# Kernel optimization log

Measured on AMD Instinct MI355X. Metric: run time of the kernel, lower is better.

The kernel has to match this reference:

```python
import jax, jax.numpy as jnp
import numpy as np

B, T, C = 4, 2048, 1024
H = 16
HD = C // H  # 64


def setup_inputs() -> dict:
    key = jax.random.key(0)
    k1, k2, k3 = jax.random.split(key, 3)
    x = jax.random.normal(k1, (B, T, C), dtype=jnp.float32)
    # learned params (torch Linear y = x @ W.T stored here as [in, out])
    Wqkv = jax.random.normal(k2, (C, 3 * C), dtype=jnp.float32) * (C ** -0.5)
    Wout = jax.random.normal(k3, (C, C), dtype=jnp.float32) * (C ** -0.5)
    bout = jnp.zeros((C,), dtype=jnp.float32)
    causal_mask = jnp.tril(jnp.ones((1, 1, T, T), dtype=bool))
    return {"x": x, "causal_mask": causal_mask, "Wqkv": Wqkv, "Wout": Wout, "bout": bout}


def reference(x, causal_mask, Wqkv, Wout, bout):
    b, t, c = x.shape
    scale = HD ** -0.5
    qkv = x @ Wqkv  # [B,T,3C]
    q, k, v = jnp.split(qkv, 3, axis=-1)
    # [B,T,C] -> [B,H,T,hd]
    q = q.reshape(b, t, H, HD).transpose(0, 2, 1, 3)
    k = k.reshape(b, t, H, HD).transpose(0, 2, 1, 3)
    v = v.reshape(b, t, H, HD).transpose(0, 2, 1, 3)
    att = jnp.einsum("bhqd,bhkd->bhqk", q, k) * scale  # [B,H,T,T]
    att = jnp.where(causal_mask, att, -jnp.inf)
    att = jax.nn.softmax(att, axis=-1)
    # dropout in eval mode == identity
    out = jnp.einsum("bhqk,bhkd->bhqd", att, v)  # [B,H,T,hd]
    out = out.transpose(0, 2, 1, 3).reshape(b, t, c)
    return out @ Wout + bout


if __name__ == "__main__":
    inp = setup_inputs()
    y = jax.jit(reference)(**inp)
    print(y.shape, y.dtype)
```

## Files before the change

kernel.cpp:

```cpp
#include <hip/hip_runtime.h>
#include <hip/hip_bf16.h>
#include <stdint.h>


typedef __bf16 bf16;
typedef __bf16 bf16x4 __attribute__((ext_vector_type(4)));
typedef __bf16 bf16x8 __attribute__((ext_vector_type(8)));
typedef float floatx4 __attribute__((ext_vector_type(4)));

#define MFMA16(a, b, c) __builtin_amdgcn_mfma_f32_16x16x32_bf16(a, b, c, 0, 0, 0)

#if defined(__has_builtin)
#if __has_builtin(__builtin_amdgcn_global_load_lds)
#define HAS_GLL 1
#endif
#endif

#ifdef HAS_GLL
__device__ __forceinline__ void gll16(const bf16* g, bf16* l) {
  __builtin_amdgcn_global_load_lds(
      (const __attribute__((address_space(1))) unsigned int*)g,
      (__attribute__((address_space(3))) unsigned int*)l, 16, 0, 0);
}
#endif

__global__ __launch_bounds__(256)
void convert_x(const float* __restrict__ in, bf16* __restrict__ out) {
  const size_t i = (size_t)blockIdx.x * 256 + threadIdx.x;
  const float4* p = (const float4*)in + i * 2;
  float4 a = p[0], b = p[1];
  bf16x8 v;
  v[0] = (bf16)a.x; v[1] = (bf16)a.y; v[2] = (bf16)a.z; v[3] = (bf16)a.w;
  v[4] = (bf16)b.x; v[5] = (bf16)b.y; v[6] = (bf16)b.z; v[7] = (bf16)b.w;
  *((bf16x8*)out + i) = v;
}

__global__ __launch_bounds__(256)
void transpose_w(const float* __restrict__ W, bf16* __restrict__ Wt, int K, int N) {
  __shared__ bf16 tile[32][33];
  const int k0 = blockIdx.y * 32, n0 = blockIdx.x * 32;
  const int t = threadIdx.x;
  {
    const int r = t >> 3, c4 = (t & 7) * 4;
    float4 v = *(const float4*)(W + (size_t)(k0 + r) * N + n0 + c4);
    tile[r][c4 + 0] = (bf16)v.x;
    tile[r][c4 + 1] = (bf16)v.y;
    tile[r][c4 + 2] = (bf16)v.z;
    tile[r][c4 + 3] = (bf16)v.w;
  }
  __syncthreads();
  {
    const int nr = t >> 3, kc = (t & 7) * 4;
    bf16x4 o;
#pragma unroll
    for (int j = 0; j < 4; ++j) o[j] = tile[kc + j][nr];
    *(bf16x4*)(Wt + (size_t)(n0 + nr) * K + k0 + kc) = o;
  }
}

__global__ __launch_bounds__(256)
void vtrans(const bf16* __restrict__ qkv, bf16* __restrict__ vtp) {
  __shared__ bf16 tile[64][72];
  const int t = threadIdx.x;
  const int kb = blockIdx.x * 64;
  const int bh = blockIdx.y;
  const int b = bh >> 4, h = bh & 15;
  const bf16* Vp = qkv + (size_t)b * 2048 * 3072 + 2048 + h * 64;
#pragma unroll
  for (int i = 0; i < 2; ++i) {
    const int c = t + 256 * i, kk = c >> 3, dg = c & 7;
    *(bf16x8*)(&tile[kk][dg * 8]) =
        *(const bf16x8*)(Vp + (size_t)(kb + kk) * 3072 + dg * 8);
  }
  __syncthreads();
#pragma unroll
  for (int i = 0; i < 2; ++i) {
    const int c = t + 256 * i, d = c >> 3, g = c & 7;
    bf16x8 v;
#pragma unroll
    for (int j = 0; j < 8; ++j) v[j] = tile[g * 8 + j][d];
    *(bf16x8*)(vtp + ((size_t)bh * 64 + d) * 2048 + kb + g * 8) = v;
  }
}

template <bool OUT_BF16>
__global__ __launch_bounds__(256, 3)
void gemm_bt(const bf16* __restrict__ A, const bf16* __restrict__ Bt,
             const float* __restrict__ bias, void* __restrict__ Cv,
             int M, int N, int K) {
  __shared__ __align__(16) bf16 As[128 * 64];
  __shared__ __align__(16) bf16 Bs[128 * 64];

  const int t = threadIdx.x, lane = t & 63, w = t >> 6;
  const int m_ = lane & 15, quad = lane >> 4;
  const int wm = w >> 1, wn = w & 1;
  const int m0 = blockIdx.y * 128, n0 = blockIdx.x * 128;

  floatx4 acc[4][4];
#pragma unroll
  for (int i = 0; i < 4; ++i)
#pragma unroll
    for (int j = 0; j < 4; ++j) {
      floatx4 z = {0.f, 0.f, 0.f, 0.f};
      acc[i][j] = z;
    }

  for (int k0 = 0; k0 < K; k0 += 64) {
#pragma unroll
    for (int i = 0; i < 4; ++i) {
      const int R0 = i * 32 + w * 8;
      const int R = R0 + (lane >> 3);
      const int sg = (lane & 7) ^ (R & 7);
      const bf16* ga = A + (size_t)(m0 + R) * K + k0 + sg * 8;
      const bf16* gb = Bt + (size_t)(n0 + R) * K + k0 + sg * 8;
#ifdef HAS_GLL
      gll16(ga, As + (size_t)R0 * 64);
      gll16(gb, Bs + (size_t)R0 * 64);
#else
      *(bf16x8*)(As + (size_t)R * 64 + (lane & 7) * 8) = *(const bf16x8*)ga;
      *(bf16x8*)(Bs + (size_t)R * 64 + (lane & 7) * 8) = *(const bf16x8*)gb;
#endif
    }
    __syncthreads();

#pragma unroll
    for (int kc = 0; kc < 2; ++kc) {
      bf16x8 af[4], bfr[4];
#pragma unroll
      for (int mt = 0; mt < 4; ++mt) {
        const int r = wm * 64 + mt * 16 + m_;
        const int slot = ((kc << 2) | quad) ^ (r & 7);
        af[mt] = *(const bf16x8*)(As + (size_t)r * 64 + slot * 8);
      }
#pragma unroll
      for (int nt = 0; nt < 4; ++nt) {
        const int rn = wn * 64 + nt * 16 + m_;
        const int slot = ((kc << 2) | quad) ^ (rn & 7);
        bfr[nt] = *(const bf16x8*)(Bs + (size_t)rn * 64 + slot * 8);
      }
#pragma unroll
      for (int mt = 0; mt < 4; ++mt)
#pragma unroll
        for (int nt = 0; nt < 4; ++nt)
          acc[mt][nt] = MFMA16(af[mt], bfr[nt], acc[mt][nt]);
    }
    __syncthreads();
  }

#pragma unroll
  for (int mt = 0; mt < 4; ++mt)
#pragma unroll
    for (int nt = 0; nt < 4; ++nt) {
      const int col = n0 + wn * 64 + nt * 16 + m_;
      const float bv = bias ? bias[col] : 0.f;
#pragma unroll
      for (int r = 0; r < 4; ++r) {
        const int row = m0 + wm * 64 + mt * 16 + quad * 4 + r;
        const float val = acc[mt][nt][r] + bv;
        if (OUT_BF16)
          ((bf16*)Cv)[(size_t)row * N + col] = (bf16)val;
        else
          ((float*)Cv)[(size_t)row * N + col] = val;
      }
    }
}

__global__ __launch_bounds__(256, 2)
void attn_fwd(const bf16* __restrict__ qkv, const bf16* __restrict__ vtp,
              bf16* __restrict__ attnout) {
  constexpr int KS = 72;
  __shared__ __align__(16) bf16 Ks[64 * KS];
  __shared__ __align__(16) bf16 VT[64 * KS];
  __shared__ __align__(16) bf16 Pl[128 * KS];

  const int t = threadIdx.x, lane = t & 63, w = t >> 6;
  const int m_ = lane & 15, quad = lane >> 4;
  const int pb = blockIdx.x;
  const int bh = blockIdx.y;
  const int b = bh >> 4, h = bh & 15;
  const int srcbase = (lane & 48) + ((lane & 48) >> 2);

  const bf16* base = qkv + (size_t)b * 2048 * 3072;
  const bf16* Qp = base + h * 64;
  const bf16* Kp = base + 1024 + h * 64;
  const bf16* Vt = vtp + (size_t)bh * 64 * 2048;

#pragma unroll
  for (int pass = 0; pass < 2; ++pass) {
    const int qb = pass ? (15 - pb) : pb;
    const int q0w = qb * 128 + w * 32;

    bf16x8 qf[2][2];
#pragma unroll
    for (int mt = 0; mt < 2; ++mt)
#pragma unroll
      for (int kc = 0; kc < 2; ++kc)
        qf[mt][kc] = *(const bf16x8*)(Qp + (size_t)(q0w + mt * 16 + m_) * 3072 +
                                      kc * 32 + quad * 8);

    floatx4 o[2][4];
#pragma unroll
    for (int mt = 0; mt < 2; ++mt)
#pragma unroll
      for (int nt = 0; nt < 4; ++nt) {
        floatx4 z = {0.f, 0.f, 0.f, 0.f};
        o[mt][nt] = z;
      }
    float mrow[2] = {-1e30f, -1e30f}, lrow[2] = {0.f, 0.f};

    const int nch = 2 * qb + 2;
    for (int ch = 0; ch < nch; ++ch) {
      const int kb = ch * 64;
#pragma unroll
      for (int i = 0; i < 2; ++i) {
        const int c = t + 256 * i, r8 = c >> 3, g = c & 7;
        *(bf16x8*)(Ks + (size_t)r8 * KS + g * 8) =
            *(const bf16x8*)(Kp + (size_t)(kb + r8) * 3072 + g * 8);
        *(bf16x8*)(VT + (size_t)r8 * KS + g * 8) =
            *(const bf16x8*)(Vt + (size_t)r8 * 2048 + kb + g * 8);
      }
      __syncthreads();

      if (kb <= q0w + 31) {
        bf16x8 kf[4][2];
#pragma unroll
        for (int kt = 0; kt < 4; ++kt)
#pragma unroll
          for (int kc = 0; kc < 2; ++kc)
            kf[kt][kc] = *(const bf16x8*)(Ks + (size_t)(kt * 16 + m_) * KS +
                                          kc * 32 + quad * 8);
        const bool need_mask = (kb + 63 > q0w);
#pragma unroll
        for (int mt = 0; mt < 2; ++mt) {
          floatx4 s[4];
#pragma unroll
          for (int kt = 0; kt < 4; ++kt) {
            floatx4 z = {0.f, 0.f, 0.f, 0.f};
            z = MFMA16(kf[kt][0], qf[mt][0], z);
            z = MFMA16(kf[kt][1], qf[mt][1], z);
            s[kt] = z;
          }
          const int qglob = q0w + mt * 16 + m_;
          float a[4][4];
          float mx = -1e30f;
#pragma unroll
          for (int kt = 0; kt < 4; ++kt)
#pragma unroll
            for (int r = 0; r < 4; ++r) {
              float v = s[kt][r] * 0.125f;
              if (need_mask && (kb + kt * 16 + quad * 4 + r > qglob)) v = -1e30f;
              a[kt][r] = v;
              mx = fmaxf(mx, v);
            }
          mx = fmaxf(mx, __shfl_xor(mx, 16));
          mx = fmaxf(mx, __shfl_xor(mx, 32));
          const float mnew = fmaxf(mrow[mt], mx);
          const float alpha = __expf(mrow[mt] - mnew);
          mrow[mt] = mnew;
          float psum = 0.f;
#pragma unroll
          for (int kt = 0; kt < 4; ++kt) {
            bf16x4 pw;
#pragma unroll
            for (int r = 0; r < 4; ++r) {
              const float p = __expf(a[kt][r] - mnew);
              psum += p;
              pw[r] = (bf16)p;
            }
            *(bf16x4*)(Pl + (size_t)((w * 2 + mt) * 16 + m_) * KS + kt * 16 +
                       quad * 4) = pw;
          }
          psum += __shfl_xor(psum, 16);
          psum += __shfl_xor(psum, 32);
          lrow[mt] = lrow[mt] * alpha + psum;
#pragma unroll
          for (int r = 0; r < 4; ++r) {
            const float ar = __shfl(alpha, srcbase + r);
#pragma unroll
            for (int nt = 0; nt < 4; ++nt) o[mt][nt][r] *= ar;
          }
        }
        bf16x8 vf[4][2];
#pragma unroll
        for (int nt = 0; nt < 4; ++nt)
#pragma unroll
          for (int kc = 0; kc < 2; ++kc)
            vf[nt][kc] = *(const bf16x8*)(VT + (size_t)(nt * 16 + m_) * KS +
                                          kc * 32 + quad * 8);
#pragma unroll
        for (int mt = 0; mt < 2; ++mt) {
          const bf16* prow = Pl + (size_t)((w * 2 + mt) * 16 + m_) * KS;
          const bf16x8 pf0 = *(const bf16x8*)(prow + quad * 8);
          const bf16x8 pf1 = *(const bf16x8*)(prow + 32 + quad * 8);
#pragma unroll
          for (int nt = 0; nt < 4; ++nt) {
            o[mt][nt] = MFMA16(pf0, vf[nt][0], o[mt][nt]);
            o[mt][nt] = MFMA16(pf1, vf[nt][1], o[mt][nt]);
          }
        }
      }
      __syncthreads();
    }

#pragma unroll
    for (int mt = 0; mt < 2; ++mt) {
      const float linv = 1.0f / lrow[mt];
#pragma unroll
      for (int r = 0; r < 4; ++r) {
        const float inv = __shfl(linv, srcbase + r);
        const int row = q0w + mt * 16 + quad * 4 + r;
        const size_t orow = ((size_t)b * 2048 + row) * 1024 + h * 64;
#pragma unroll
        for (int nt = 0; nt < 4; ++nt)
          attnout[orow + nt * 16 + m_] = (bf16)(o[mt][nt][r] * inv);
      }
    }
  }
}

extern "C" void kernel_launch(void* const* d_in, const int* in_sizes, int n_in,
                              void* d_out, int out_size, void* d_ws, size_t ws_size,
                              hipStream_t stream) {
  (void)in_sizes; (void)n_in; (void)out_size; (void)ws_size;
  const float* x    = (const float*)d_in[0];
  const float* Wqkv = (const float*)d_in[2];
  const float* Wout = (const float*)d_in[3];
  const float* bout = (const float*)d_in[4];
  float* out = (float*)d_out;

  bf16* qkv     = (bf16*)d_ws;
  bf16* attnout = (bf16*)((char*)d_ws + (size_t)8192 * 3072 * 2);
  bf16* Wout_t  = (bf16*)d_ws;
  bf16* xbf    = (bf16*)d_out;
  bf16* Wqkv_t = (bf16*)d_out + (size_t)8192 * 1024;
  bf16* vtp    = (bf16*)d_out + (size_t)8192 * 1024;

  convert_x<<<4096, 256, 0, stream>>>(x, xbf);
  transpose_w<<<dim3(96, 32), 256, 0, stream>>>(Wqkv, Wqkv_t, 1024, 3072);

  gemm_bt<true><<<dim3(24, 64), 256, 0, stream>>>(xbf, Wqkv_t, nullptr, qkv,
                                                  8192, 3072, 1024);
  vtrans<<<dim3(32, 64), 256, 0, stream>>>(qkv, vtp);
  attn_fwd<<<dim3(8, 64), 256, 0, stream>>>(qkv, vtp, attnout);

  transpose_w<<<dim3(32, 32), 256, 0, stream>>>(Wout, Wout_t, 1024, 1024);
  gemm_bt<false><<<dim3(8, 64), 256, 0, stream>>>(attnout, Wout_t, bout, out,
                                                  8192, 1024, 1024);
}
```

Baseline: 299.1 us.

## Prefetch next K/V chunk into registers and use exp2 softmax in attention

The attention kernel now loads the next 64-key K and V^T chunk into registers while the current chunk is being computed, then writes those registers to LDS between two barriers. This hides global load latency behind the MFMA and softmax work. The scale is pre-multiplied by log2(e) so exp2f replaces __expf, and the causal mask is applied in a separate branch. The grid axes are swapped so that blocks sharing a (b,h) pair are no longer adjacent in launch order, which changes L2 locality. The cost is higher register pressure and an extra barrier per chunk.

```diff
diff --git a/kernel.cpp b/kernel.cpp
--- a/kernel.cpp
+++ b/kernel.cpp
@@ -169,14 +169,15 @@
 void attn_fwd(const bf16* __restrict__ qkv, const bf16* __restrict__ vtp,
               bf16* __restrict__ attnout) {
   constexpr int KS = 72;
+  constexpr float L2E = 1.44269504f;
   __shared__ __align__(16) bf16 Ks[64 * KS];
   __shared__ __align__(16) bf16 VT[64 * KS];
   __shared__ __align__(16) bf16 Pl[128 * KS];
 
   const int t = threadIdx.x, lane = t & 63, w = t >> 6;
   const int m_ = lane & 15, quad = lane >> 4;
-  const int pb = blockIdx.x;
-  const int bh = blockIdx.y;
+  const int bh = blockIdx.x;
+  const int pb = blockIdx.y;
   const int b = bh >> 4, h = bh & 15;
   const int srcbase = (lane & 48) + ((lane & 48) >> 2);
 
@@ -185,6 +186,9 @@
   const bf16* Kp = base + 1024 + h * 64;
   const bf16* Vt = vtp + (size_t)bh * 64 * 2048;
 
+  const int sr0 = t >> 3, sg0 = t & 7;
+  const int sr1 = (t + 256) >> 3, sg1 = t & 7;
+
 #pragma unroll
   for (int pass = 0; pass < 2; ++pass) {
     const int qb = pass ? (15 - pb) : pb;
@@ -209,17 +213,28 @@
     float mrow[2] = {-1e30f, -1e30f}, lrow[2] = {0.f, 0.f};
 
     const int nch = 2 * qb + 2;
+
+    bf16x8 kr0, kr1, vr0, vr1;
+    kr0 = *(const bf16x8*)(Kp + (size_t)sr0 * 3072 + sg0 * 8);
+    kr1 = *(const bf16x8*)(Kp + (size_t)sr1 * 3072 + sg1 * 8);
+    vr0 = *(const bf16x8*)(Vt + (size_t)sr0 * 2048 + sg0 * 8);
+    vr1 = *(const bf16x8*)(Vt + (size_t)sr1 * 2048 + sg1 * 8);
+
     for (int ch = 0; ch < nch; ++ch) {
       const int kb = ch * 64;
-#pragma unroll
-      for (int i = 0; i < 2; ++i) {
-        const int c = t + 256 * i, r8 = c >> 3, g = c & 7;
-        *(bf16x8*)(Ks + (size_t)r8 * KS + g * 8) =
-            *(const bf16x8*)(Kp + (size_t)(kb + r8) * 3072 + g * 8);
-        *(bf16x8*)(VT + (size_t)r8 * KS + g * 8) =
-            *(const bf16x8*)(Vt + (size_t)r8 * 2048 + kb + g * 8);
-      }
       __syncthreads();
+      *(bf16x8*)(Ks + (size_t)sr0 * KS + sg0 * 8) = kr0;
+      *(bf16x8*)(Ks + (size_t)sr1 * KS + sg1 * 8) = kr1;
+      *(bf16x8*)(VT + (size_t)sr0 * KS + sg0 * 8) = vr0;
+      *(bf16x8*)(VT + (size_t)sr1 * KS + sg1 * 8) = vr1;
+      __syncthreads();
+      if (ch + 1 < nch) {
+        const int kn = kb + 64;
+        kr0 = *(const bf16x8*)(Kp + (size_t)(kn + sr0) * 3072 + sg0 * 8);
+        kr1 = *(const bf16x8*)(Kp + (size_t)(kn + sr1) * 3072 + sg1 * 8);
+        vr0 = *(const bf16x8*)(Vt + (size_t)sr0 * 2048 + kn + sg0 * 8);
+        vr1 = *(const bf16x8*)(Vt + (size_t)sr1 * 2048 + kn + sg1 * 8);
+      }
 
       if (kb <= q0w + 31) {
         bf16x8 kf[4][2];
@@ -240,22 +255,28 @@
             z = MFMA16(kf[kt][1], qf[mt][1], z);
             s[kt] = z;
           }
-          const int qglob = q0w + mt * 16 + m_;
           float a[4][4];
+#pragma unroll
+          for (int kt = 0; kt < 4; ++kt)
+#pragma unroll
+            for (int r = 0; r < 4; ++r) a[kt][r] = s[kt][r] * (0.125f * L2E);
+          if (need_mask) {
+            const int qglob = q0w + mt * 16 + m_;
+#pragma unroll
+            for (int kt = 0; kt < 4; ++kt)
+#pragma unroll
+              for (int r = 0; r < 4; ++r)
+                if (kb + kt * 16 + quad * 4 + r > qglob) a[kt][r] = -1e30f;
+          }
           float mx = -1e30f;
 #pragma unroll
           for (int kt = 0; kt < 4; ++kt)
 #pragma unroll
-            for (int r = 0; r < 4; ++r) {
-              float v = s[kt][r] * 0.125f;
-              if (need_mask && (kb + kt * 16 + quad * 4 + r > qglob)) v = -1e30f;
-              a[kt][r] = v;
-              mx = fmaxf(mx, v);
-            }
+            for (int r = 0; r < 4; ++r) mx = fmaxf(mx, a[kt][r]);
           mx = fmaxf(mx, __shfl_xor(mx, 16));
           mx = fmaxf(mx, __shfl_xor(mx, 32));
           const float mnew = fmaxf(mrow[mt], mx);
-          const float alpha = __expf(mrow[mt] - mnew);
+          const float alpha = exp2f(mrow[mt] - mnew);
           mrow[mt] = mnew;
           float psum = 0.f;
 #pragma unroll
@@ -263,7 +284,7 @@
             bf16x4 pw;
 #pragma unroll
             for (int r = 0; r < 4; ++r) {
-              const float p = __expf(a[kt][r] - mnew);
+              const float p = exp2f(a[kt][r] - mnew);
               psum += p;
               pw[r] = (bf16)p;
             }
@@ -299,8 +320,8 @@
           }
         }
       }
-      __syncthreads();
-    }
+    }
+    __syncthreads();
 
 #pragma unroll
     for (int mt = 0; mt < 2; ++mt) {
@@ -341,7 +362,7 @@
   gemm_bt<true><<<dim3(24, 64), 256, 0, stream>>>(xbf, Wqkv_t, nullptr, qkv,
                                                   8192, 3072, 1024);
   vtrans<<<dim3(32, 64), 256, 0, stream>>>(qkv, vtp);
-  attn_fwd<<<dim3(8, 64), 256, 0, stream>>>(qkv, vtp, attnout);
+  attn_fwd<<<dim3(64, 8), 256, 0, stream>>>(qkv, vtp, attnout);
 
   transpose_w<<<dim3(32, 32), 256, 0, stream>>>(Wout, Wout_t, 1024, 1024);
   gemm_bt<false><<<dim3(8, 64), 256, 0, stream>>>(attnout, Wout_t, bout, out,
```

After: 281.9 us. -5.7%, faster.
